# Kernel optimization log

Measured on AMD Instinct MI355X. Metric: run time of the kernel, lower is better.

Reference implementation:

```python
import jax, jax.numpy as jnp
import numpy as np

NEG_INF = -1e9  # matches torch masked_fill value -1000000000.0
K = 3  # Conv1d kernel size


def setup_inputs() -> dict:
    key = jax.random.key(0)
    k1, k2, k3, k4 = jax.random.split(key, 4)
    B, V, F, H = 128, 200, 64, 128
    input_visit = jax.random.normal(k1, (B, V, F), dtype=jnp.float32)
    visit_mask = jax.random.randint(k2, (B, 1, V - K + 1), 0, 2, dtype=jnp.int32)
    # per-feature Conv1d(1, H, 3) weights stacked: [F, H, K], bias [F, H]
    fan_in = 1 * K
    bound = 1.0 / np.sqrt(fan_in)
    conv_w = jax.random.uniform(k3, (F, H, K), dtype=jnp.float32, minval=-bound, maxval=bound)
    conv_b = jax.random.uniform(k4, (F, H), dtype=jnp.float32, minval=-bound, maxval=bound)
    return {"input_visit": input_visit, "visit_mask": visit_mask, "conv_w": conv_w, "conv_b": conv_b}


def reference(input_visit, visit_mask, conv_w, conv_b):
    # input_visit: [B, V, F]; visit_mask: [B, 1, L] with L = V-K+1
    B, V, F = input_visit.shape
    L = V - K + 1
    x = jnp.transpose(input_visit, (0, 2, 1))  # [B, F, V]
    # sliding windows: [B, F, L, K]
    win = jnp.stack([x[:, :, k:k + L] for k in range(K)], axis=-1)
    # per-feature conv (in_channels=1): [B, F, H, L]
    conv = jnp.einsum('bflk,fhk->bfhl', win, conv_w) + conv_b[None, :, :, None]
    # masked_fill where mask == 0, broadcast [B,1,1,L] -> [B,F,H,L]
    masked = jnp.where(visit_mask[:, None, :, :] == 0, NEG_INF, conv)
    # max over time -> [B, F, H] (== torch.cat of per-feature outputs along dim=1)
    return jnp.max(masked, axis=-1)
```

## Files before the change

kernel.cpp:

```cpp
#include <hip/hip_runtime.h>


#define NEG_INF_F (-1e9f)

constexpr int B_ = 128;
constexpr int V_ = 200;
constexpr int F_ = 64;
constexpr int H_ = 128;
constexpr int K_ = 3;
constexpr int L_ = V_ - K_ + 1;

constexpr int FG = 8;
constexpr int NTHR = 256;
constexpr int HPT = 4;

__global__ __launch_bounds__(NTHR)
void fve_kernel(const float* __restrict__ x,
                const int*   __restrict__ mask,
                const float* __restrict__ w,
                const float* __restrict__ bias,
                float* __restrict__ out)
{
    __shared__ float xs[FG][V_ + 1];
    __shared__ int   vlist[L_];
    __shared__ int   vcnt;

    const int b  = blockIdx.x >> 3;
    const int fg = blockIdx.x & 7;
    const int f0 = fg * FG;
    const int t  = threadIdx.x;

    if (t == 0) vcnt = 0;
    __syncthreads();

    for (int idx = t; idx < V_ * 2; idx += NTHR) {
        const int v = idx >> 1, half = idx & 1;
        const float4 vec = *reinterpret_cast<const float4*>(
            x + ((size_t)b * V_ + v) * F_ + f0 + half * 4);
        const int fl = half * 4;
        xs[fl + 0][v] = vec.x;
        xs[fl + 1][v] = vec.y;
        xs[fl + 2][v] = vec.z;
        xs[fl + 3][v] = vec.w;
    }

    for (int l = t; l < L_; l += NTHR) {
        if (mask[b * L_ + l] != 0) {
            const int p = atomicAdd(&vcnt, 1);
            vlist[p] = l;
        }
    }
    __syncthreads();

    const int f_local = t >> 5;
    const int f       = f0 + f_local;
    const int h0      = (t & 31) * HPT;

    const float* wp = w + ((size_t)f * H_ + h0) * K_;
    const float4 w0 = *reinterpret_cast<const float4*>(wp);
    const float4 w1 = *reinterpret_cast<const float4*>(wp + 4);
    const float4 w2 = *reinterpret_cast<const float4*>(wp + 8);
    const float4 bb = *reinterpret_cast<const float4*>(bias + (size_t)f * H_ + h0);

    float m0 = NEG_INF_F, m1 = NEG_INF_F, m2 = NEG_INF_F, m3 = NEG_INF_F;
    const int n = vcnt;
    for (int i = 0; i < n; ++i) {
        const int l = vlist[i];
        const float x0 = xs[f_local][l];
        const float x1 = xs[f_local][l + 1];
        const float x2 = xs[f_local][l + 2];
        const float c0 = fmaf(x0, w0.x, fmaf(x1, w0.y, fmaf(x2, w0.z, bb.x)));
        const float c1 = fmaf(x0, w0.w, fmaf(x1, w1.x, fmaf(x2, w1.y, bb.y)));
        const float c2 = fmaf(x0, w1.z, fmaf(x1, w1.w, fmaf(x2, w2.x, bb.z)));
        const float c3 = fmaf(x0, w2.y, fmaf(x1, w2.z, fmaf(x2, w2.w, bb.w)));
        m0 = fmaxf(m0, c0);
        m1 = fmaxf(m1, c1);
        m2 = fmaxf(m2, c2);
        m3 = fmaxf(m3, c3);
    }

    *reinterpret_cast<float4*>(out + ((size_t)b * F_ + f) * H_ + h0) =
        make_float4(m0, m1, m2, m3);
}

extern "C" void kernel_launch(void* const* d_in, const int* in_sizes, int n_in,
                              void* d_out, int out_size, void* d_ws, size_t ws_size,
                              hipStream_t stream) {
    const float* x    = (const float*)d_in[0];
    const int*   mask = (const int*)d_in[1];
    const float* w    = (const float*)d_in[2];
    const float* bias = (const float*)d_in[3];
    float* out = (float*)d_out;

    const int grid = B_ * (F_ / FG);
    fve_kernel<<<grid, NTHR, 0, stream>>>(x, mask, w, bias, out);
}
```

Baseline: 17.26 us.

## Compute eight hidden units per thread and sixteen features per block

Each thread now produces 8 output channels instead of 4, so every shared-memory read of the three input values feeds twice as many FMAs. Each block now covers 16 features rather than 8, which halves the grid, and each thread stages 24 weights in registers. The valid-index list is read four entries at a time through int4 loads. In exchange, register pressure rises and there are fewer blocks to spread across the CUs.

```diff
diff --git a/kernel.cpp b/kernel.cpp
--- a/kernel.cpp
+++ b/kernel.cpp
@@ -7,12 +7,13 @@
 constexpr int V_ = 200;
 constexpr int F_ = 64;
 constexpr int H_ = 128;
-constexpr int K_ = 3;
-constexpr int L_ = V_ - K_ + 1;
+constexpr int L_ = V_ - 3 + 1;
 
-constexpr int FG = 8;
 constexpr int NTHR = 256;
-constexpr int HPT = 4;
+constexpr int HPT  = 8;
+constexpr int TPF  = H_ / HPT;
+constexpr int FG   = NTHR / TPF;
+constexpr int XSTR = 204;
 
 __global__ __launch_bounds__(NTHR)
 void fve_kernel(const float* __restrict__ x,
@@ -21,23 +22,22 @@
                 const float* __restrict__ bias,
                 float* __restrict__ out)
 {
-    __shared__ float xs[FG][V_ + 1];
-    __shared__ int   vlist[L_];
-    __shared__ int   vcnt;
+    __shared__ __align__(16) float xs[FG][XSTR];
+    __shared__ __align__(16) int   vlist[((L_ + 3) / 4) * 4];
+    __shared__ int vcnt;
 
-    const int b  = blockIdx.x >> 3;
-    const int fg = blockIdx.x & 7;
-    const int f0 = fg * FG;
+    const int b  = blockIdx.x >> 2;
+    const int f0 = (blockIdx.x & 3) * FG;
     const int t  = threadIdx.x;
 
     if (t == 0) vcnt = 0;
     __syncthreads();
 
-    for (int idx = t; idx < V_ * 2; idx += NTHR) {
-        const int v = idx >> 1, half = idx & 1;
+    for (int idx = t; idx < V_ * 4; idx += NTHR) {
+        const int v = idx >> 2, q = idx & 3;
         const float4 vec = *reinterpret_cast<const float4*>(
-            x + ((size_t)b * V_ + v) * F_ + f0 + half * 4);
-        const int fl = half * 4;
+            x + ((size_t)b * V_ + v) * F_ + f0 + q * 4);
+        const int fl = q * 4;
         xs[fl + 0][v] = vec.x;
         xs[fl + 1][v] = vec.y;
         xs[fl + 2][v] = vec.z;
@@ -52,35 +52,58 @@
     }
     __syncthreads();
 
-    const int f_local = t >> 5;
+    const int f_local = t >> 4;
     const int f       = f0 + f_local;
-    const int h0      = (t & 31) * HPT;
+    const int h0      = (t & 15) * HPT;
 
-    const float* wp = w + ((size_t)f * H_ + h0) * K_;
-    const float4 w0 = *reinterpret_cast<const float4*>(wp);
-    const float4 w1 = *reinterpret_cast<const float4*>(wp + 4);
-    const float4 w2 = *reinterpret_cast<const float4*>(wp + 8);
-    const float4 bb = *reinterpret_cast<const float4*>(bias + (size_t)f * H_ + h0);
+    const float* wp = w + ((size_t)f * H_ + h0) * 3;
+    float wt[24];
+#pragma unroll
+    for (int j = 0; j < 6; ++j)
+        *reinterpret_cast<float4*>(&wt[j * 4]) =
+            *reinterpret_cast<const float4*>(wp + j * 4);
 
-    float m0 = NEG_INF_F, m1 = NEG_INF_F, m2 = NEG_INF_F, m3 = NEG_INF_F;
-    const int n = vcnt;
-    for (int i = 0; i < n; ++i) {
-        const int l = vlist[i];
-        const float x0 = xs[f_local][l];
-        const float x1 = xs[f_local][l + 1];
-        const float x2 = xs[f_local][l + 2];
-        const float c0 = fmaf(x0, w0.x, fmaf(x1, w0.y, fmaf(x2, w0.z, bb.x)));
-        const float c1 = fmaf(x0, w0.w, fmaf(x1, w1.x, fmaf(x2, w1.y, bb.y)));
-        const float c2 = fmaf(x0, w1.z, fmaf(x1, w1.w, fmaf(x2, w2.x, bb.z)));
-        const float c3 = fmaf(x0, w2.y, fmaf(x1, w2.z, fmaf(x2, w2.w, bb.w)));
-        m0 = fmaxf(m0, c0);
-        m1 = fmaxf(m1, c1);
-        m2 = fmaxf(m2, c2);
-        m3 = fmaxf(m3, c3);
+    float bb[8];
+    *reinterpret_cast<float4*>(&bb[0]) =
+        *reinterpret_cast<const float4*>(bias + (size_t)f * H_ + h0);
+    *reinterpret_cast<float4*>(&bb[4]) =
+        *reinterpret_cast<const float4*>(bias + (size_t)f * H_ + h0 + 4);
+
+    float m[8];
+#pragma unroll
+    for (int hh = 0; hh < 8; ++hh) m[hh] = NEG_INF_F;
+
+    const float* row = &xs[f_local][0];
+    const int n  = vcnt;
+    const int n4 = n & ~3;
+    const int4* vq = reinterpret_cast<const int4*>(vlist);
+
+#define PROC(lv)                                                              \
+    do {                                                                      \
+        const int   l  = (lv);                                                \
+        const float x0 = row[l], x1 = row[l + 1], x2 = row[l + 2];            \
+        _Pragma("unroll")                                                     \
+        for (int hh = 0; hh < 8; ++hh) {                                      \
+            const float c = fmaf(x0, wt[3 * hh],                              \
+                            fmaf(x1, wt[3 * hh + 1],                          \
+                            fmaf(x2, wt[3 * hh + 2], bb[hh])));               \
+            m[hh] = fmaxf(m[hh], c);                                          \
+        }                                                                     \
+    } while (0)
+
+    for (int i = 0; i < n4; i += 4) {
+        const int4 ls = vq[i >> 2];
+        PROC(ls.x);
+        PROC(ls.y);
+        PROC(ls.z);
+        PROC(ls.w);
     }
+    for (int i = n4; i < n; ++i) PROC(vlist[i]);
+#undef PROC
 
-    *reinterpret_cast<float4*>(out + ((size_t)b * F_ + f) * H_ + h0) =
-        make_float4(m0, m1, m2, m3);
+    float* op = out + ((size_t)b * F_ + f) * H_ + h0;
+    *reinterpret_cast<float4*>(op)     = make_float4(m[0], m[1], m[2], m[3]);
+    *reinterpret_cast<float4*>(op + 4) = make_float4(m[4], m[5], m[6], m[7]);
 }
 
 extern "C" void kernel_launch(void* const* d_in, const int* in_sizes, int n_in,
```

After: 17.77 us. +2.9%, slower.
